# Optimization experiments

Measured on AMD Instinct MI355X. Metric: run time of the kernel, lower is better.

## Reference

```python
import jax, jax.numpy as jnp
import numpy as np
import math

EPS = 1e-5

def _layernorm(x, g, b):
    m = x.mean(-1, keepdims=True)
    v = ((x - m) ** 2).mean(-1, keepdims=True)
    return (x - m) / jnp.sqrt(v + EPS) * g + b

def _skew(emd):
    # RelativePositionalEmbed pad/cat/view skew trick. emd: (B,H,S,S)
    B, H, S, _ = emd.shape
    x = jnp.concatenate([emd, jnp.zeros_like(emd)], -1)   # (B,H,S,2S)
    x = x.reshape(B, H, -1)                                # (B,H,2*S*S)
    l = 2 * S - 1
    extra = (-x.shape[-1]) % l
    x = jnp.concatenate([x, jnp.zeros((B, H, extra), x.dtype)], -1)
    x = x.reshape(B, H, -1, l)
    return x[..., :S, S - 1:]                              # (B,H,S,S)

def setup_inputs() -> dict:
    key = jax.random.key(0)
    ks = jax.random.split(key, 8)
    S, B, D, H, DFF = 1024, 4, 1024, 16, 4096
    dh = D // H
    sc = 1.0 / math.sqrt(D)
    return {
        'x': jax.random.normal(ks[0], (S, B, D), jnp.float32),
        'wq': jax.random.normal(ks[1], (D, D), jnp.float32) * sc,
        'wk': jax.random.normal(ks[2], (D, D), jnp.float32) * sc,
        'wv': jax.random.normal(ks[3], (D, D), jnp.float32) * sc,
        'rel_w': jax.random.normal(ks[4], (B, H, dh, S), jnp.float32) * (1.0 / math.sqrt(dh)),
        'ln1_g': jnp.ones((D,), jnp.float32),
        'ln1_b': jnp.zeros((D,), jnp.float32),
        'ln2_g': jnp.ones((D,), jnp.float32),
        'ln2_b': jnp.zeros((D,), jnp.float32),
        'w1_w': jax.random.normal(ks[5], (DFF, D), jnp.float32) * sc,
        'w1_b': jnp.zeros((DFF,), jnp.float32),
        'w2_w': jax.random.normal(ks[6], (D, DFF), jnp.float32) * (1.0 / math.sqrt(DFF)),
        'w2_b': jnp.zeros((D,), jnp.float32),
    }

def reference(x, wq, wk, wv, rel_w, ln1_g, ln1_b, ln2_g, ln2_b, w1_w, w1_b, w2_w, w2_b):
    S, B, D = x.shape
    H = rel_w.shape[1]
    dh = D // H

    def proj(w):
        y = x @ w.T                      # (S,B,D)
        # torch .view(B,S,H,dh): raw row-major reinterpretation, not a transpose
        return y.reshape(B, S, H, dh).swapaxes(1, 2)  # (B,H,S,dh)

    q, k, v = proj(wq), proj(wk), proj(wv)
    scores = jnp.einsum('bhsd,bhtd->bhst', q * (1.0 / math.sqrt(dh)), k)  # (B,H,S,S)
    # mask=False path: the on-the-fly linear1/linear2 reprojection of qk is
    # computed then discarded in the original; omitted here (dead code).
    emd = jnp.einsum('bhsd,bhdt->bhst', q, rel_w)
    scores = scores + _skew(emd)
    attn = jax.nn.softmax(scores, axis=0)            # softmax over BATCH dim, as in source
    out = jnp.einsum('bhst,bhtd->bhsd', attn, v)     # (B,H,S,dh)
    attn_out = out.reshape(S, B, D)                  # raw reshape, as in source
    h1 = _layernorm(x + attn_out, ln1_g, ln1_b)      # dropout = identity (eval)
    ffn = jnp.maximum(h1 @ w1_w.T + w1_b, 0.0) @ w2_w.T + w2_b
    return _layernorm(h1 + ffn, ln2_g, ln2_b)
```

## Files before the change

### kernel.cpp

```cpp
#include <hip/hip_runtime.h>


typedef unsigned short u16;
typedef unsigned int u32;
typedef __attribute__((ext_vector_type(4))) float f32x4;
typedef __attribute__((ext_vector_type(8))) short bf16x8;
typedef __attribute__((ext_vector_type(4))) u32 u32x4;

__device__ __forceinline__ float bf2f(u16 u) { return __uint_as_float(((u32)u) << 16); }
__device__ __forceinline__ u16 f2bf(float f) {
    u32 u = __float_as_uint(f);
    u += 0x7fffu + ((u >> 16) & 1u);
    return (u16)(u >> 16);
}
template<int DT>
__device__ __forceinline__ float load1(const void* P, size_t idx) {
    return (DT == 0) ? bf2f(((const u16*)P)[idx]) : ((const float*)P)[idx];
}

#define GL16(gp, lp)                                                        \
    __builtin_amdgcn_global_load_lds(                                       \
        (const __attribute__((address_space(1))) void*)(gp),                \
        (__attribute__((address_space(3))) void*)(lp), 16, 0, 0)

__global__ __launch_bounds__(256) void sentinel_ws(float* out, u32 n)
{
    for (u32 i = blockIdx.x * 256 + threadIdx.x; i < n; i += gridDim.x * 256) out[i] = 31000.0f;
}

__global__ __launch_bounds__(256) void cvt_f32_bf16(const float* __restrict__ s,
                                                    u16* __restrict__ d, u32 n)
{
    u32 i = (blockIdx.x * 256 + threadIdx.x) * 4;
    if (i >= n) return;
    float4 v = *(const float4*)(s + i);
    uint2 pk;
    pk.x = (u32)f2bf(v.x) | ((u32)f2bf(v.y) << 16);
    pk.y = (u32)f2bf(v.z) | ((u32)f2bf(v.w) << 16);
    *(uint2*)(d + i) = pk;
}

__global__ __launch_bounds__(256) void relw_tr(const float* __restrict__ relw,
                                               u16* __restrict__ relwT)
{
    __shared__ __align__(16) float T[64][68];
    const int tid = threadIdx.x;
    const int bh = blockIdx.y;
    const int u0 = blockIdx.x << 6;
    {
        const int d = tid >> 2, uq = (tid & 3) << 4;
        const float* rp = relw + (size_t)bh * 65536 + (size_t)d * 1024 + u0 + uq;
#pragma unroll
        for (int i = 0; i < 4; i++)
            *(float4*)&T[d][uq + i * 4] = *(const float4*)(rp + i * 4);
    }
    __syncthreads();
    {
        const int u = tid >> 2, dq = (tid & 3) << 4;
        u32 pk[8];
#pragma unroll
        for (int p = 0; p < 8; p++) {
            float a = T[dq + p * 2][u], b = T[dq + p * 2 + 1][u];
            pk[p] = (u32)f2bf(a) | ((u32)f2bf(b) << 16);
        }
        u16* op = relwT + ((size_t)(bh * 1024 + u0 + u) << 6) + dq;
        *(uint4*)op = *(uint4*)&pk[0];
        *(uint4*)(op + 8) = *(uint4*)&pk[4];
    }
}

__global__ __launch_bounds__(256) void yv_tr(const u16* __restrict__ Yv,
                                             u16* __restrict__ YvT)
{
    __shared__ __align__(16) u16 T[64][72];
    const int tid = threadIdx.x;
    const int bh = blockIdx.y, b = bh >> 4, h = bh & 15;
    const int t0 = blockIdx.x << 6;
    {
        const int r = tid >> 2, cq = (tid & 3) << 4;
        const u16* p = Yv + ((size_t)(b * 1024 + t0 + r) << 10) + h * 64 + cq;
        *(uint4*)&T[r][cq] = *(const uint4*)p;
        *(uint4*)&T[r][cq + 8] = *(const uint4*)(p + 8);
    }
    __syncthreads();
    {
        const int d = tid >> 2, tq = (tid & 3) << 4;
        u16 vals[16];
#pragma unroll
        for (int p = 0; p < 16; p++) vals[p] = T[tq + p][d];
        u16* op = YvT + (((size_t)bh * 64 + d) << 10) + t0 + tq;
        *(uint4*)op = ((uint4*)vals)[0];
        *(uint4*)(op + 8) = ((uint4*)vals)[1];
    }
}

template<int RELU, int OUT_F32, int HAS_BIAS, int SPLIT3, int STAGE,
         int CHX, int CHY>
__global__ __launch_bounds__(256) void mfma_gemm(
    const u16* __restrict__ A, const u16* __restrict__ B,
    const float* __restrict__ bias, void* __restrict__ Cout,
    int M, int N, int K)
{
    __shared__ __align__(16) u16 As[8192];
    __shared__ __align__(16) u16 Bs[8192];
    const int tid = threadIdx.x;
    const int wave = tid >> 6, lane = tid & 63;
    const int quad = lane >> 4, l16 = lane & 15;

    constexpr int S = CHX * CHY;
    const int l = blockIdx.y * gridDim.x + blockIdx.x;
    const int j = l >> 3;
    const int c = (l & 7) + ((j / S) << 3);
    const int w = j % S;
    const int nxc = gridDim.x / CHX;
    const int bx = (c % nxc) * CHX + (w % CHX);
    const int by = (c / nxc) * CHY + (w / CHX);
    const int m0 = by << 7, n0 = bx << 7;
    const int wm = (wave >> 1) << 6, wn = (wave & 1) << 6;

    f32x4 acc[4][4];
#pragma unroll
    for (int i = 0; i < 4; i++)
#pragma unroll
        for (int jj = 0; jj < 4; jj++) acc[i][jj] = (f32x4){0.f, 0.f, 0.f, 0.f};

    if (STAGE) {
        const int srow = tid >> 3;
        const int csw = ((tid & 7) ^ ((tid >> 3) & 7)) << 3;
        const u16* Ags = A + (size_t)(m0 + srow) * K + csw;
        const u16* Bgs = B + (size_t)(n0 + srow) * K + csw;
        const int rx = (l16 & 7) << 3;

        for (int k0 = 0; k0 < K; k0 += 64) {
            __syncthreads();
#pragma unroll
            for (int i = 0; i < 4; i++) {
                GL16(Ags + (size_t)(i * 32) * K + k0, &As[(i * 256 + tid) * 8]);
                GL16(Bgs + (size_t)(i * 32) * K + k0, &Bs[(i * 256 + tid) * 8]);
            }
            __syncthreads();

#pragma unroll
            for (int kk = 0; kk < 2; kk++) {
                bf16x8 af[4], bfr[4];
#pragma unroll
                for (int mi = 0; mi < 4; mi++)
                    af[mi] = *(const bf16x8*)(As + ((wm + mi * 16 + l16) << 6) +
                                              ((((kk * 4 + quad) << 3) ^ rx)));
#pragma unroll
                for (int ni = 0; ni < 4; ni++)
                    bfr[ni] = *(const bf16x8*)(Bs + ((wn + ni * 16 + l16) << 6) +
                                               ((((kk * 4 + quad) << 3) ^ rx)));
#pragma unroll
                for (int mi = 0; mi < 4; mi++)
#pragma unroll
                    for (int ni = 0; ni < 4; ni++)
                        acc[mi][ni] = __builtin_amdgcn_mfma_f32_16x16x32_bf16(
                            af[mi], bfr[ni], acc[mi][ni], 0, 0, 0);
            }
        }
    } else {
        const int r0 = tid >> 2;
        const int csw = ((tid & 3) ^ ((r0 >> 1) & 3)) << 3;
        const u16* Ag0 = A + (size_t)(m0 + r0) * K + csw;
        const u16* Ag1 = A + (size_t)(m0 + r0 + 64) * K + csw;
        const u16* Bg0 = B + (size_t)(n0 + r0) * K + csw;
        const u16* Bg1 = B + (size_t)(n0 + r0 + 64) * K + csw;
        const int pb = ((quad ^ ((l16 >> 1) & 3)) << 3);

        uint4 a0 = *(const uint4*)(Ag0);
        uint4 a1 = *(const uint4*)(Ag1);
        uint4 b0 = *(const uint4*)(Bg0);
        uint4 b1 = *(const uint4*)(Bg1);

        for (int k0 = 0; k0 < K; k0 += 32) {
            __syncthreads();
            *(uint4*)(As + tid * 8)        = a0;
            *(uint4*)(As + 2048 + tid * 8) = a1;
            *(uint4*)(Bs + tid * 8)        = b0;
            *(uint4*)(Bs + 2048 + tid * 8) = b1;
            __syncthreads();

            if (k0 + 32 < K) {
                a0 = *(const uint4*)(Ag0 + k0 + 32);
                a1 = *(const uint4*)(Ag1 + k0 + 32);
                b0 = *(const uint4*)(Bg0 + k0 + 32);
                b1 = *(const uint4*)(Bg1 + k0 + 32);
            }

            bf16x8 af[4], bfr[4];
#pragma unroll
            for (int mi = 0; mi < 4; mi++)
                af[mi] = *(const bf16x8*)(As + ((wm + mi * 16 + l16) << 5) + pb);
#pragma unroll
            for (int ni = 0; ni < 4; ni++)
                bfr[ni] = *(const bf16x8*)(Bs + ((wn + ni * 16 + l16) << 5) + pb);
#pragma unroll
            for (int mi = 0; mi < 4; mi++)
#pragma unroll
                for (int ni = 0; ni < 4; ni++)
                    acc[mi][ni] = __builtin_amdgcn_mfma_f32_16x16x32_bf16(
                        af[mi], bfr[ni], acc[mi][ni], 0, 0, 0);
        }
    }

    float bb[4];
#pragma unroll
    for (int ni = 0; ni < 4; ni++)
        bb[ni] = HAS_BIAS ? bias[n0 + wn + ni * 16 + l16] : 0.f;

#pragma unroll
    for (int mi = 0; mi < 4; mi++) {
#pragma unroll
        for (int ni = 0; ni < 4; ni++) {
            const int col = n0 + wn + ni * 16 + l16;
            const size_t cb = SPLIT3
                ? (((size_t)(col >> 10) << 22) + (size_t)(col & 1023))
                : (size_t)col;
#pragma unroll
            for (int r = 0; r < 4; r++) {
                const int row = m0 + wm + mi * 16 + quad * 4 + r;
                float v = acc[mi][ni][r] + bb[ni];
                if (RELU) v = fmaxf(v, 0.f);
                const size_t idx = SPLIT3 ? (cb + ((size_t)row << 10))
                                          : ((size_t)row * N + cb);
                if (OUT_F32) ((float*)Cout)[idx] = v;
                else ((u16*)Cout)[idx] = f2bf(v);
            }
        }
    }
}

__global__ __launch_bounds__(256, 1) void attn_fused(
    const u16* __restrict__ Yq, const u16* __restrict__ Yk,
    const u16* __restrict__ relwT, const u16* __restrict__ YvT,
    float* __restrict__ O)
{
    __shared__ __align__(16) u16 lds[76288];
    u16* Ks  = lds;
    u16* Rw  = lds + 16384;
    u16* Ssh = lds + 49152;
    u16* Ebp = lds + 67584;

    const int tid = threadIdx.x;
    const int wave = tid >> 6, lane = tid & 63;
    const int quad = lane >> 4, l16 = lane & 15;
    const int ws = wave >> 1, wt = wave & 1;

    const int bid = blockIdx.x;
    const int swz = (bid & 7) * 32 + (bid >> 3);
    const int h = swz >> 4, si = swz & 15;
    const int s0 = si << 6;
    const int qb0 = 15 - si;
    const int tau0 = 2 + wt * 2 - ws * 2;
    u16* EbW = Ebp + wave * 2176;

    bf16x8 qf[4][2][2];
#pragma unroll
    for (int b = 0; b < 4; b++)
#pragma unroll
        for (int mi = 0; mi < 2; mi++)
#pragma unroll
            for (int kk = 0; kk < 2; kk++)
                qf[b][mi][kk] = *(const bf16x8*)(Yq +
                    ((size_t)(b * 1024 + s0 + ws * 32 + mi * 16 + l16) << 10) +
                    h * 64 + kk * 32 + quad * 8);

    f32x4 acc[4][4];
#pragma unroll
    for (int b = 0; b < 4; b++)
#pragma unroll
        for (int nj = 0; nj < 4; nj++) acc[b][nj] = (f32x4){0.f, 0.f, 0.f, 0.f};

    auto phase2 = [&](int t0p) {
#pragma unroll
        for (int kk = 0; kk < 2; kk++) {
            u32x4 pcf[4];
#pragma unroll
            for (int b = 0; b < 4; b++)
                pcf[b] = *(const u32x4*)(Ssh + b * 4608 +
                                         (wave * 16 + l16) * 72 + kk * 32 + quad * 8);
            u32x4 aw[4];
#pragma unroll
            for (int j = 0; j < 4; j++) {
                float x0[4], x1[4];
#pragma unroll
                for (int b = 0; b < 4; b++) {
                    const u32 wd = pcf[b][j];
                    x0[b] = __uint_as_float(wd << 16);
                    x1[b] = __uint_as_float(wd & 0xffff0000u);
                }
                const float m0 = fmaxf(fmaxf(x0[0], x0[1]), fmaxf(x0[2], x0[3]));
                const float m1 = fmaxf(fmaxf(x1[0], x1[1]), fmaxf(x1[2], x1[3]));
                float s0v = 0.f, s1v = 0.f;
#pragma unroll
                for (int b = 0; b < 4; b++) {
                    x0[b] = __expf(x0[b] - m0); s0v += x0[b];
                    x1[b] = __expf(x1[b] - m1); s1v += x1[b];
                }
                const float r0 = 1.f / s0v, r1 = 1.f / s1v;
#pragma unroll
                for (int b = 0; b < 4; b++)
                    aw[b][j] = (u32)f2bf(x0[b] * r0) | ((u32)f2bf(x1[b] * r1) << 16);
            }
#pragma unroll
            for (int b = 0; b < 4; b++) {
                const bf16x8 af = __builtin_bit_cast(bf16x8, aw[b]);
#pragma unroll
                for (int nj = 0; nj < 4; nj++) {
                    bf16x8 bv = *(const bf16x8*)(YvT +
                        ((size_t)(b * 16 + h) << 16) + ((size_t)(nj * 16 + l16) << 10) +
                        t0p + kk * 32 + quad * 8);
                    acc[b][nj] = __builtin_amdgcn_mfma_f32_16x16x32_bf16(
                        af, bv, acc[b][nj], 0, 0, 0);
                }
            }
        }
    };

    for (int i = 0; i < 16; i++) {
        const int t0 = i << 6;

#pragma unroll
        for (int k = 0; k < 2; k++) {
            const int idx = k * 256 + tid;
            const int row = idx >> 3;
            const int csw = ((idx & 7) ^ (row & 7)) << 3;
#pragma unroll
            for (int b = 0; b < 4; b++)
                GL16(Yk + ((size_t)(b * 1024 + t0 + row) << 10) + h * 64 + csw,
                     Ks + b * 4096 + idx * 8);
        }
        if (i == 0) {
#pragma unroll
            for (int k = 0; k < 2; k++) {
                const int idx = k * 256 + tid;
                const int row = idx >> 3;
                const int csw = ((idx & 7) ^ (row & 7)) << 3;
#pragma unroll
                for (int b = 0; b < 4; b++)
                    GL16(relwT + ((size_t)((b * 16 + h) * 1024 + 960 - s0 + row) << 6) + csw,
                         Rw + (b * 2 + (qb0 & 1)) * 4096 + idx * 8);
            }
        }
        if (i <= si) {
            const int sl2 = (qb0 + i + 1) & 1;
#pragma unroll
            for (int k = 0; k < 2; k++) {
                const int idx = k * 256 + tid;
                const int row = idx >> 3;
                const int csw = ((idx & 7) ^ (row & 7)) << 3;
                const int u = 1024 - s0 + t0 + row;
#pragma unroll
                for (int b = 0; b < 4; b++) {
                    u16* dst = Rw + (b * 2 + sl2) * 4096 + idx * 8;
                    if (u < 1024)
                        GL16(relwT + ((size_t)((b * 16 + h) * 1024 + u) << 6) + csw, dst);
                    else
                        *(u32x4*)dst = (u32x4){0, 0, 0, 0};
                }
            }
        }

        if (i) phase2(t0 - 64);
        __syncthreads();

        const int eact = (i <= si);
        const int qb = qb0 + i;
#pragma unroll
        for (int b = 0; b < 4; b++) {
            f32x4 aqk[2][2];
#pragma unroll
            for (int mi = 0; mi < 2; mi++)
#pragma unroll
                for (int nj = 0; nj < 2; nj++) aqk[mi][nj] = (f32x4){0.f, 0.f, 0.f, 0.f};
#pragma unroll
            for (int kk = 0; kk < 2; kk++)
#pragma unroll
                for (int nj = 0; nj < 2; nj++) {
                    const int tr = wt * 32 + nj * 16 + l16;
                    bf16x8 kb = *(const bf16x8*)(Ks + b * 4096 + tr * 64 +
                                                 (((kk * 4 + quad) ^ (tr & 7)) << 3));
#pragma unroll
                    for (int mi = 0; mi < 2; mi++)
                        aqk[mi][nj] = __builtin_amdgcn_mfma_f32_16x16x32_bf16(
                            qf[b][mi][kk], kb, aqk[mi][nj], 0, 0, 0);
                }

            if (eact) {
                f32x4 ae[4][2];
#pragma unroll
                for (int uj = 0; uj < 4; uj++)
#pragma unroll
                    for (int mi = 0; mi < 2; mi++) ae[uj][mi] = (f32x4){0.f, 0.f, 0.f, 0.f};
#pragma unroll
                for (int kk = 0; kk < 2; kk++)
#pragma unroll
                    for (int uj = 0; uj < 4; uj++) {
                        const int tau = tau0 + uj;
                        const int ur = (tau & 3) * 16 + l16;
                        const u16* hp = Rw + (b * 2 + ((qb + (tau >> 2)) & 1)) * 4096;
                        bf16x8 ra = *(const bf16x8*)(hp + ur * 64 +
                                                     (((kk * 4 + quad) ^ (ur & 7)) << 3));
#pragma unroll
                        for (int mi = 0; mi < 2; mi++)
                            ae[uj][mi] = __builtin_amdgcn_mfma_f32_16x16x32_bf16(
                                ra, qf[b][mi][kk], ae[uj][mi], 0, 0, 0);
                    }
#pragma unroll
                for (int uj = 0; uj < 4; uj++)
#pragma unroll
                    for (int mi = 0; mi < 2; mi++) {
                        const int rloc = mi * 16 + l16;
                        const int cb = uj * 16 + quad * 4;
                        uint2 pk;
                        pk.x = (u32)f2bf(ae[uj][mi][0]) | ((u32)f2bf(ae[uj][mi][1]) << 16);
                        pk.y = (u32)f2bf(ae[uj][mi][2]) | ((u32)f2bf(ae[uj][mi][3]) << 16);
                        *(uint2*)(EbW + rloc * 68 + cb) = pk;
                    }
            }

#pragma unroll
            for (int mi = 0; mi < 2; mi++)
#pragma unroll
                for (int nj = 0; nj < 2; nj++)
#pragma unroll
                    for (int rr = 0; rr < 4; rr++) {
                        const int slq = mi * 16 + quad * 4 + rr;
                        const int sl = ws * 32 + slq;
                        const int tl = wt * 32 + nj * 16 + l16;
                        float e = 0.f;
                        if (eact)
                            e = bf2f(EbW[slq * 68 + 31 + nj * 16 + l16 -
                                         mi * 16 - quad * 4 - rr]);
                        Ssh[b * 4608 + sl * 72 + tl] =
                            f2bf(aqk[mi][nj][rr] * 0.125f + e);
                    }
        }
        __syncthreads();
    }
    phase2(960);

#pragma unroll
    for (int b = 0; b < 4; b++)
#pragma unroll
        for (int nj = 0; nj < 4; nj++)
#pragma unroll
            for (int rr = 0; rr < 4; rr++) {
                const int row = s0 + wave * 16 + quad * 4 + rr;
                O[((((size_t)(b * 16 + h) << 10) + row) << 6) + nj * 16 + l16] =
                    acc[b][nj][rr];
            }
}

template<int DTA, int OUT_F32>
__global__ __launch_bounds__(256) void add_ln(
    const void* __restrict__ A, const float* __restrict__ Bf,
    const float* __restrict__ g, const float* __restrict__ beta,
    void* __restrict__ out)
{
    const int row = blockIdx.x;
    const int tid = threadIdx.x;
    const size_t base = (size_t)row * 1024;
    float v[4], s1 = 0.f, s2 = 0.f;
#pragma unroll
    for (int k = 0; k < 4; k++) {
        const int c = k * 256 + tid;
        float t = load1<DTA>(A, base + c) + Bf[base + c];
        v[k] = t; s1 += t; s2 += t * t;
    }
#pragma unroll
    for (int m = 1; m < 64; m <<= 1) {
        s1 += __shfl_xor(s1, m, 64);
        s2 += __shfl_xor(s2, m, 64);
    }
    __shared__ float red[8];
    if ((tid & 63) == 0) { red[(tid >> 6) * 2] = s1; red[(tid >> 6) * 2 + 1] = s2; }
    __syncthreads();
    s1 = red[0] + red[2] + red[4] + red[6];
    s2 = red[1] + red[3] + red[5] + red[7];
    const float mean = s1 * (1.f / 1024.f);
    const float var = s2 * (1.f / 1024.f) - mean * mean;
    const float rstd = rsqrtf(var + 1e-5f);
#pragma unroll
    for (int k = 0; k < 4; k++) {
        const int c = k * 256 + tid;
        float o = (v[k] - mean) * rstd * g[c] + beta[c];
        if (OUT_F32) ((float*)out)[base + c] = o;
        else ((u16*)out)[base + c] = f2bf(o);
    }
}

extern "C" void kernel_launch(void* const* d_in, const int* in_sizes, int n_in,
                              void* d_out, int out_size, void* d_ws, size_t ws_size,
                              hipStream_t stream)
{
    const float* x    = (const float*)d_in[0];
    const float* wq   = (const float*)d_in[1];
    const float* wk   = (const float*)d_in[2];
    const float* wv   = (const float*)d_in[3];
    const float* relw = (const float*)d_in[4];
    const float* g1   = (const float*)d_in[5];
    const float* be1  = (const float*)d_in[6];
    const float* g2   = (const float*)d_in[7];
    const float* be2  = (const float*)d_in[8];
    const float* w1   = (const float*)d_in[9];
    const float* b1   = (const float*)d_in[10];
    const float* w2   = (const float*)d_in[11];
    const float* b2   = (const float*)d_in[12];

    const size_t NEEDED = ((size_t)224 << 20);
    if (ws_size < NEEDED) {
        sentinel_ws<<<dim3(1024), dim3(256), 0, stream>>>((float*)d_out, (u32)out_size);
        return;
    }

    char* ws = (char*)d_ws;
    float* O     = (float*)(ws);
    u16*   Yq    = (u16*)(ws + ((size_t)16 << 20));
    u16*   Yk    = (u16*)(ws + ((size_t)24 << 20));
    u16*   Yv    = (u16*)(ws + ((size_t)32 << 20));
    u16*   h1    = (u16*)(ws + ((size_t)40 << 20));
    u16*   ffn1  = (u16*)(ws + ((size_t)48 << 20));
    float* ffn2  = (float*)(ws + ((size_t)80 << 20));
    u16*   YvT   = (u16*)(ws + ((size_t)80 << 20));
    u16*   xb    = (u16*)(ws + ((size_t)96 << 20));
    u16*   wqb   = (u16*)(ws + ((size_t)104 << 20));
    u16*   wkb   = (u16*)(ws + ((size_t)106 << 20));
    u16*   wvb   = (u16*)(ws + ((size_t)108 << 20));
    u16*   relwT = (u16*)(ws + ((size_t)112 << 20));
    u16*   w1b   = (u16*)(ws + ((size_t)96 << 20));
    u16*   w2b   = (u16*)(ws + ((size_t)104 << 20));

    dim3 blk(256);
    const u32 M4 = 4u << 20, M1 = 1u << 20;

    cvt_f32_bf16<<<dim3(M4 / 1024), blk, 0, stream>>>(x,  xb,  M4);
    cvt_f32_bf16<<<dim3(M1 / 1024), blk, 0, stream>>>(wq, wqb, M1);
    cvt_f32_bf16<<<dim3(M1 / 1024), blk, 0, stream>>>(wk, wkb, M1);
    cvt_f32_bf16<<<dim3(M1 / 1024), blk, 0, stream>>>(wv, wvb, M1);
    relw_tr<<<dim3(16, 64), blk, 0, stream>>>(relw, relwT);

    mfma_gemm<0,0,0,1,1,12,8><<<dim3(24, 32), blk, 0, stream>>>(
        xb, wqb, nullptr, Yq, 4096, 3072, 1024);
    yv_tr<<<dim3(16, 64), blk, 0, stream>>>(Yv, YvT);

    attn_fused<<<dim3(256), blk, 0, stream>>>(Yq, Yk, relwT, YvT, O);

    add_ln<1,0><<<dim3(4096), blk, 0, stream>>>(x, O, g1, be1, h1);

    cvt_f32_bf16<<<dim3(M4 / 1024), blk, 0, stream>>>(w1, w1b, M4);
    cvt_f32_bf16<<<dim3(M4 / 1024), blk, 0, stream>>>(w2, w2b, M4);

    mfma_gemm<1,0,1,0,1,8,16><<<dim3(32, 32), blk, 0, stream>>>(h1, w1b, b1, ffn1, 4096, 4096, 1024);
    mfma_gemm<0,1,1,0,0,4,8><<<dim3(8, 32), blk, 0, stream>>>(ffn1, w2b, b2, ffn2, 4096, 1024, 4096);

    add_ln<0,1><<<dim3(4096), blk, 0, stream>>>(h1, ffn2, g2, be2, (float*)d_out);
}
```

Baseline: 486.1 us.

## Split fused attention work across 8 waves per block instead of 4

Doubles the attention block to 512 threads, so each wave owns one 16-row query strip and half of the key/value columns. Per-wave QK, relative-embedding and PV work shrinks, the redundant rel-embed tile drops from 4 to 3 per wave, and the global-to-LDS loads are spread over more threads. This aims to hide latency with more waves per CU, since only 256 blocks run. The cost is the softmax work in phase2 now being duplicated across the two column-half waves, plus a different LDS scratch layout.

```diff
diff --git a/kernel.cpp b/kernel.cpp
--- a/kernel.cpp
+++ b/kernel.cpp
@@ -231,12 +231,12 @@
     }
 }
 
-__global__ __launch_bounds__(256, 1) void attn_fused(
+__global__ __launch_bounds__(512, 1) void attn_fused(
     const u16* __restrict__ Yq, const u16* __restrict__ Yk,
     const u16* __restrict__ relwT, const u16* __restrict__ YvT,
     float* __restrict__ O)
 {
-    __shared__ __align__(16) u16 lds[76288];
+    __shared__ __align__(16) u16 lds[74240];
     u16* Ks  = lds;
     u16* Rw  = lds + 16384;
     u16* Ssh = lds + 49152;
@@ -245,32 +245,30 @@
     const int tid = threadIdx.x;
     const int wave = tid >> 6, lane = tid & 63;
     const int quad = lane >> 4, l16 = lane & 15;
-    const int ws = wave >> 1, wt = wave & 1;
+    const int g4 = wave >> 1, g2 = wave & 1;
 
     const int bid = blockIdx.x;
     const int swz = (bid & 7) * 32 + (bid >> 3);
     const int h = swz >> 4, si = swz & 15;
     const int s0 = si << 6;
     const int qb0 = 15 - si;
-    const int tau0 = 2 + wt * 2 - ws * 2;
-    u16* EbW = Ebp + wave * 2176;
-
-    bf16x8 qf[4][2][2];
+    const int tau0w = 3 + 2 * g2 - g4;
+    u16* EbW = Ebp + wave * 832;
+
+    bf16x8 qf[4][2];
 #pragma unroll
     for (int b = 0; b < 4; b++)
 #pragma unroll
-        for (int mi = 0; mi < 2; mi++)
-#pragma unroll
-            for (int kk = 0; kk < 2; kk++)
-                qf[b][mi][kk] = *(const bf16x8*)(Yq +
-                    ((size_t)(b * 1024 + s0 + ws * 32 + mi * 16 + l16) << 10) +
-                    h * 64 + kk * 32 + quad * 8);
-
-    f32x4 acc[4][4];
+        for (int kk = 0; kk < 2; kk++)
+            qf[b][kk] = *(const bf16x8*)(Yq +
+                ((size_t)(b * 1024 + s0 + g4 * 16 + l16) << 10) +
+                h * 64 + kk * 32 + quad * 8);
+
+    f32x4 acc[4][2];
 #pragma unroll
     for (int b = 0; b < 4; b++)
 #pragma unroll
-        for (int nj = 0; nj < 4; nj++) acc[b][nj] = (f32x4){0.f, 0.f, 0.f, 0.f};
+        for (int nj = 0; nj < 2; nj++) acc[b][nj] = (f32x4){0.f, 0.f, 0.f, 0.f};
 
     auto phase2 = [&](int t0p) {
 #pragma unroll
@@ -279,7 +277,7 @@
 #pragma unroll
             for (int b = 0; b < 4; b++)
                 pcf[b] = *(const u32x4*)(Ssh + b * 4608 +
-                                         (wave * 16 + l16) * 72 + kk * 32 + quad * 8);
+                                         (g4 * 16 + l16) * 72 + kk * 32 + quad * 8);
             u32x4 aw[4];
 #pragma unroll
             for (int j = 0; j < 4; j++) {
@@ -307,58 +305,44 @@
             for (int b = 0; b < 4; b++) {
                 const bf16x8 af = __builtin_bit_cast(bf16x8, aw[b]);
 #pragma unroll
-                for (int nj = 0; nj < 4; nj++) {
+                for (int njl = 0; njl < 2; njl++) {
+                    const int nj = g2 * 2 + njl;
                     bf16x8 bv = *(const bf16x8*)(YvT +
                         ((size_t)(b * 16 + h) << 16) + ((size_t)(nj * 16 + l16) << 10) +
                         t0p + kk * 32 + quad * 8);
-                    acc[b][nj] = __builtin_amdgcn_mfma_f32_16x16x32_bf16(
-                        af, bv, acc[b][nj], 0, 0, 0);
+                    acc[b][njl] = __builtin_amdgcn_mfma_f32_16x16x32_bf16(
+                        af, bv, acc[b][njl], 0, 0, 0);
                 }
             }
         }
     };
+
+    const int vrow = tid >> 3;
+    const int vcsw = ((tid & 7) ^ (vrow & 7)) << 3;
 
     for (int i = 0; i < 16; i++) {
         const int t0 = i << 6;
 
 #pragma unroll
-        for (int k = 0; k < 2; k++) {
-            const int idx = k * 256 + tid;
-            const int row = idx >> 3;
-            const int csw = ((idx & 7) ^ (row & 7)) << 3;
+        for (int b = 0; b < 4; b++)
+            GL16(Yk + ((size_t)(b * 1024 + t0 + vrow) << 10) + h * 64 + vcsw,
+                 Ks + b * 4096 + tid * 8);
+        if (i == 0) {
 #pragma unroll
             for (int b = 0; b < 4; b++)
-                GL16(Yk + ((size_t)(b * 1024 + t0 + row) << 10) + h * 64 + csw,
-                     Ks + b * 4096 + idx * 8);
-        }
-        if (i == 0) {
-#pragma unroll
-            for (int k = 0; k < 2; k++) {
-                const int idx = k * 256 + tid;
-                const int row = idx >> 3;
-                const int csw = ((idx & 7) ^ (row & 7)) << 3;
-#pragma unroll
-                for (int b = 0; b < 4; b++)
-                    GL16(relwT + ((size_t)((b * 16 + h) * 1024 + 960 - s0 + row) << 6) + csw,
-                         Rw + (b * 2 + (qb0 & 1)) * 4096 + idx * 8);
-            }
+                GL16(relwT + ((size_t)((b * 16 + h) * 1024 + 960 - s0 + vrow) << 6) + vcsw,
+                     Rw + (b * 2 + (qb0 & 1)) * 4096 + tid * 8);
         }
         if (i <= si) {
             const int sl2 = (qb0 + i + 1) & 1;
-#pragma unroll
-            for (int k = 0; k < 2; k++) {
-                const int idx = k * 256 + tid;
-                const int row = idx >> 3;
-                const int csw = ((idx & 7) ^ (row & 7)) << 3;
-                const int u = 1024 - s0 + t0 + row;
-#pragma unroll
-                for (int b = 0; b < 4; b++) {
-                    u16* dst = Rw + (b * 2 + sl2) * 4096 + idx * 8;
-                    if (u < 1024)
-                        GL16(relwT + ((size_t)((b * 16 + h) * 1024 + u) << 6) + csw, dst);
-                    else
-                        *(u32x4*)dst = (u32x4){0, 0, 0, 0};
-                }
+            const int u = 1024 - s0 + t0 + vrow;
+#pragma unroll
+            for (int b = 0; b < 4; b++) {
+                u16* dst = Rw + (b * 2 + sl2) * 4096 + tid * 8;
+                if (u < 1024)
+                    GL16(relwT + ((size_t)((b * 16 + h) * 1024 + u) << 6) + vcsw, dst);
+                else
+                    *(u32x4*)dst = (u32x4){0, 0, 0, 0};
             }
         }
 
@@ -369,73 +353,58 @@
         const int qb = qb0 + i;
 #pragma unroll
         for (int b = 0; b < 4; b++) {
-            f32x4 aqk[2][2];
-#pragma unroll
-            for (int mi = 0; mi < 2; mi++)
-#pragma unroll
-                for (int nj = 0; nj < 2; nj++) aqk[mi][nj] = (f32x4){0.f, 0.f, 0.f, 0.f};
+            f32x4 aqk[2];
+#pragma unroll
+            for (int nj = 0; nj < 2; nj++) aqk[nj] = (f32x4){0.f, 0.f, 0.f, 0.f};
 #pragma unroll
             for (int kk = 0; kk < 2; kk++)
 #pragma unroll
                 for (int nj = 0; nj < 2; nj++) {
-                    const int tr = wt * 32 + nj * 16 + l16;
+                    const int tr = g2 * 32 + nj * 16 + l16;
                     bf16x8 kb = *(const bf16x8*)(Ks + b * 4096 + tr * 64 +
                                                  (((kk * 4 + quad) ^ (tr & 7)) << 3));
-#pragma unroll
-                    for (int mi = 0; mi < 2; mi++)
-                        aqk[mi][nj] = __builtin_amdgcn_mfma_f32_16x16x32_bf16(
-                            qf[b][mi][kk], kb, aqk[mi][nj], 0, 0, 0);
+                    aqk[nj] = __builtin_amdgcn_mfma_f32_16x16x32_bf16(
+                        qf[b][kk], kb, aqk[nj], 0, 0, 0);
                 }
 
             if (eact) {
-                f32x4 ae[4][2];
-#pragma unroll
-                for (int uj = 0; uj < 4; uj++)
-#pragma unroll
-                    for (int mi = 0; mi < 2; mi++) ae[uj][mi] = (f32x4){0.f, 0.f, 0.f, 0.f};
+                f32x4 ae[3];
+#pragma unroll
+                for (int uj = 0; uj < 3; uj++) ae[uj] = (f32x4){0.f, 0.f, 0.f, 0.f};
 #pragma unroll
                 for (int kk = 0; kk < 2; kk++)
 #pragma unroll
-                    for (int uj = 0; uj < 4; uj++) {
-                        const int tau = tau0 + uj;
+                    for (int uj = 0; uj < 3; uj++) {
+                        const int tau = tau0w + uj;
                         const int ur = (tau & 3) * 16 + l16;
                         const u16* hp = Rw + (b * 2 + ((qb + (tau >> 2)) & 1)) * 4096;
                         bf16x8 ra = *(const bf16x8*)(hp + ur * 64 +
                                                      (((kk * 4 + quad) ^ (ur & 7)) << 3));
-#pragma unroll
-                        for (int mi = 0; mi < 2; mi++)
-                            ae[uj][mi] = __builtin_amdgcn_mfma_f32_16x16x32_bf16(
-                                ra, qf[b][mi][kk], ae[uj][mi], 0, 0, 0);
+                        ae[uj] = __builtin_amdgcn_mfma_f32_16x16x32_bf16(
+                            ra, qf[b][kk], ae[uj], 0, 0, 0);
                     }
 #pragma unroll
-                for (int uj = 0; uj < 4; uj++)
-#pragma unroll
-                    for (int mi = 0; mi < 2; mi++) {
-                        const int rloc = mi * 16 + l16;
-                        const int cb = uj * 16 + quad * 4;
-                        uint2 pk;
-                        pk.x = (u32)f2bf(ae[uj][mi][0]) | ((u32)f2bf(ae[uj][mi][1]) << 16);
-                        pk.y = (u32)f2bf(ae[uj][mi][2]) | ((u32)f2bf(ae[uj][mi][3]) << 16);
-                        *(uint2*)(EbW + rloc * 68 + cb) = pk;
-                    }
-            }
-
-#pragma unroll
-            for (int mi = 0; mi < 2; mi++)
-#pragma unroll
-                for (int nj = 0; nj < 2; nj++)
-#pragma unroll
-                    for (int rr = 0; rr < 4; rr++) {
-                        const int slq = mi * 16 + quad * 4 + rr;
-                        const int sl = ws * 32 + slq;
-                        const int tl = wt * 32 + nj * 16 + l16;
-                        float e = 0.f;
-                        if (eact)
-                            e = bf2f(EbW[slq * 68 + 31 + nj * 16 + l16 -
-                                         mi * 16 - quad * 4 - rr]);
-                        Ssh[b * 4608 + sl * 72 + tl] =
-                            f2bf(aqk[mi][nj][rr] * 0.125f + e);
-                    }
+                for (int uj = 0; uj < 3; uj++) {
+                    const int cb = uj * 16 + quad * 4;
+                    uint2 pk;
+                    pk.x = (u32)f2bf(ae[uj][0]) | ((u32)f2bf(ae[uj][1]) << 16);
+                    pk.y = (u32)f2bf(ae[uj][2]) | ((u32)f2bf(ae[uj][3]) << 16);
+                    *(uint2*)(EbW + l16 * 52 + cb) = pk;
+                }
+            }
+
+#pragma unroll
+            for (int nj = 0; nj < 2; nj++)
+#pragma unroll
+                for (int rr = 0; rr < 4; rr++) {
+                    const int slq = quad * 4 + rr;
+                    const int sl = g4 * 16 + slq;
+                    const int tl = g2 * 32 + nj * 16 + l16;
+                    float e = 0.f;
+                    if (eact)
+                        e = bf2f(EbW[slq * 52 + 15 + nj * 16 + l16 - quad * 4 - rr]);
+                    Ssh[b * 4608 + sl * 72 + tl] = f2bf(aqk[nj][rr] * 0.125f + e);
+                }
         }
         __syncthreads();
     }
@@ -444,12 +413,13 @@
 #pragma unroll
     for (int b = 0; b < 4; b++)
 #pragma unroll
-        for (int nj = 0; nj < 4; nj++)
+        for (int njl = 0; njl < 2; njl++)
 #pragma unroll
             for (int rr = 0; rr < 4; rr++) {
-                const int row = s0 + wave * 16 + quad * 4 + rr;
-                O[((((size_t)(b * 16 + h) << 10) + row) << 6) + nj * 16 + l16] =
-                    acc[b][nj][rr];
+                const int row = s0 + g4 * 16 + quad * 4 + rr;
+                const int col = (g2 * 2 + njl) * 16 + l16;
+                O[((((size_t)(b * 16 + h) << 10) + row) << 6) + col] =
+                    acc[b][njl][rr];
             }
 }
 
@@ -545,7 +515,7 @@
         xb, wqb, nullptr, Yq, 4096, 3072, 1024);
     yv_tr<<<dim3(16, 64), blk, 0, stream>>>(Yv, YvT);
 
-    attn_fused<<<dim3(256), blk, 0, stream>>>(Yq, Yk, relwT, YvT, O);
+    attn_fused<<<dim3(256), dim3(512), 0, stream>>>(Yq, Yk, relwT, YvT, O);
 
     add_ln<1,0><<<dim3(4096), blk, 0, stream>>>(x, O, g1, be1, h1);
 
```

After: 441.9 us. 1.1x faster.
